# Optimization experiments

Hardware: AMD Instinct MI355X
Metric: run time of the kernel (lower is better)

The kernel has to match this reference:

```python
import jax, jax.numpy as jnp
import numpy as np

B, C, H, W = 4, 256, 64, 64
DQK = C // 8

def setup_inputs() -> dict:
    key = jax.random.key(0)
    ks = jax.random.split(key, 8)
    s = 0.05
    return {
        "x": jax.random.normal(ks[0], (B, C, H, W), jnp.float32),
        "Wq": jax.random.normal(ks[1], (DQK, C), jnp.float32) * s,
        "bq": jax.random.normal(ks[2], (DQK,), jnp.float32) * s,
        "Wk": jax.random.normal(ks[3], (DQK, C), jnp.float32) * s,
        "bk": jax.random.normal(ks[4], (DQK,), jnp.float32) * s,
        "Wv": jax.random.normal(ks[5], (C, C), jnp.float32) * s,
        "bv": jax.random.normal(ks[6], (C,), jnp.float32) * s,
        "gamma": jax.random.normal(ks[7], (1,), jnp.float32) * s,
    }

def reference(x, Wq, bq, Wk, bk, Wv, bv, gamma):
    b, c, h, w = x.shape
    n = h * w
    xf = x.reshape(b, c, n)                                  # (B,C,N)
    # 1x1 convs == per-pixel linear projections
    q = jnp.einsum('dc,bcn->bnd', Wq, xf) + bq               # (B,N,Dqk)
    k = jnp.einsum('dc,bcn->bdn', Wk, xf) + bk[:, None]      # (B,Dqk,N)
    v = jnp.einsum('dc,bcn->bdn', Wv, xf) + bv[:, None]      # (B,C,N)
    energy = jnp.einsum('bnd,bdm->bnm', q, k)                # (B,N,N) — NO 1/sqrt(d) scaling, matching source
    attn = jax.nn.softmax(energy, axis=-1)
    # out[b,c,m] = sum_n v[b,c,n] * attn[m,n]  (bmm(value, attn^T))
    out = jnp.einsum('bcn,bmn->bcm', v, attn).reshape(b, c, h, w)
    return gamma * out + x
```

## Files before the change

### kernel.cpp

```cpp
#include <hip/hip_runtime.h>


#define BATCH 4
#define CH    256
#define NPIX  4096
#define DQKD  32

typedef __attribute__((ext_vector_type(8))) short bf16x8;
typedef __attribute__((ext_vector_type(4))) float f32x4;

__device__ __forceinline__ unsigned pk2(float a, float b) {
    return (__float_as_uint(a) >> 16) | (__float_as_uint(b) & 0xffff0000u);
}

__global__ __launch_bounds__(256) void proj_kernel(
    const float* __restrict__ x,
    const float* __restrict__ Wq, const float* __restrict__ bq,
    const float* __restrict__ Wk, const float* __restrict__ bk,
    const float* __restrict__ Wv, const float* __restrict__ bv,
    ushort* __restrict__ qb, ushort* __restrict__ kb, ushort* __restrict__ vb)
{
    __shared__ float w_lds[32][256];
    __shared__ float b_lds[32];
    const int tid = threadIdx.x;
    const int n0  = blockIdx.x * 256;
    const int dt  = blockIdx.y;
    const int b   = blockIdx.z;

    const float* W; const float* bias;
    if (dt == 0)      { W = Wq;                              bias = bq; }
    else if (dt == 1) { W = Wk;                              bias = bk; }
    else              { W = Wv + (size_t)(dt - 2) * 32 * CH; bias = bv + (dt - 2) * 32; }

    {
        const float4* w4 = (const float4*)W;
        float4* l4 = (float4*)&w_lds[0][0];
        #pragma unroll
        for (int i = 0; i < 8; ++i) l4[tid + 256 * i] = w4[tid + 256 * i];
        if (tid < 32) b_lds[tid] = bias[tid];
    }
    __syncthreads();

    const int tn = tid & 63;
    const int td = tid >> 6;
    const int n  = n0 + tn * 4;

    float acc[8][4];
    #pragma unroll
    for (int i = 0; i < 8; ++i) {
        float bb = b_lds[td * 8 + i];
        #pragma unroll
        for (int j = 0; j < 4; ++j) acc[i][j] = bb;
    }

    const float* xb = x + (size_t)b * CH * NPIX + n;
    for (int c0 = 0; c0 < CH; c0 += 8) {
        float xr[8][4];
        #pragma unroll
        for (int cc = 0; cc < 8; ++cc) {
            float4 xv = *(const float4*)(xb + (size_t)(c0 + cc) * NPIX);
            xr[cc][0] = xv.x; xr[cc][1] = xv.y; xr[cc][2] = xv.z; xr[cc][3] = xv.w;
        }
        #pragma unroll
        for (int i = 0; i < 8; ++i) {
            #pragma unroll
            for (int h = 0; h < 2; ++h) {
                float4 w4 = *(const float4*)&w_lds[td * 8 + i][c0 + 4 * h];
                float wr[4] = {w4.x, w4.y, w4.z, w4.w};
                #pragma unroll
                for (int cc = 0; cc < 4; ++cc)
                    #pragma unroll
                    for (int j = 0; j < 4; ++j)
                        acc[i][j] = fmaf(wr[cc], xr[4 * h + cc][j], acc[i][j]);
            }
        }
    }

    if (dt == 0 || dt == 1) {
        ushort* dst = (dt == 0) ? qb : kb;
        const float sc = (dt == 0) ? 1.4426950408889634f : 1.0f;
        #pragma unroll
        for (int j = 0; j < 4; ++j) {
            uint4 u;
            u.x = pk2(acc[0][j] * sc, acc[1][j] * sc);
            u.y = pk2(acc[2][j] * sc, acc[3][j] * sc);
            u.z = pk2(acc[4][j] * sc, acc[5][j] * sc);
            u.w = pk2(acc[6][j] * sc, acc[7][j] * sc);
            *(uint4*)(dst + ((size_t)b * NPIX + n + j) * DQKD + td * 8) = u;
        }
    } else {
        const int cbase = (dt - 2) * 32 + td * 8;
        #pragma unroll
        for (int i = 0; i < 8; ++i) {
            uint2 u;
            u.x = pk2(acc[i][0], acc[i][1]);
            u.y = pk2(acc[i][2], acc[i][3]);
            *(uint2*)(vb + ((size_t)b * CH + cbase + i) * NPIX + n) = u;
        }
    }
}

__global__ __launch_bounds__(512, 2) void attn_kernel(
    const ushort* __restrict__ Qb, const ushort* __restrict__ Kb,
    const ushort* __restrict__ Vb, const float* __restrict__ x,
    const float* __restrict__ gamma_p, float* __restrict__ out)
{
    __shared__ char  p_lds[64 * 1024];
    __shared__ float l_lds[8][64];
    __shared__ float linv_lds[64];

    const int tid  = threadIdx.x;
    const int lane = tid & 63;
    const int wv   = tid >> 6;
    const int l15  = lane & 15, g = lane >> 4;
    const unsigned swz = (unsigned)(l15 & 7) << 4;

    int bid  = blockIdx.x;
    int xcd  = bid & 7, slot = bid >> 3;
    int b    = xcd >> 1;
    int qt   = slot + 32 * (xcd & 1);
    const int m0 = qt * 64;

    bf16x8 qf[4];
    #pragma unroll
    for (int qc = 0; qc < 4; ++qc)
        qf[qc] = *(const bf16x8*)(Qb + ((size_t)b * NPIX + m0 + 16 * qc + l15) * DQKD + 8 * g);

    const ushort* kbase = Kb + ((size_t)b * NPIX + 64 * wv + l15) * DQKD + 8 * g;

    const int qh = wv >> 2;
    const int cg = wv & 3;
    const ushort* vbase = Vb + ((size_t)(b * CH + 64 * cg) + l15) * NPIX + 8 * g;

    f32x4 acc[2][4];
    #pragma unroll
    for (int q2 = 0; q2 < 2; ++q2)
        #pragma unroll
        for (int ct = 0; ct < 4; ++ct) acc[q2][ct] = (f32x4){0.f, 0.f, 0.f, 0.f};
    float l_run[4] = {0.f, 0.f, 0.f, 0.f};

    const f32x4 z4 = {0.f, 0.f, 0.f, 0.f};

    bf16x8 kc[4];
    #pragma unroll
    for (int t = 0; t < 4; ++t)
        kc[t] = *(const bf16x8*)(kbase + (size_t)(16 * t) * DQKD);

    #pragma unroll 1
    for (int kt = 0; kt < NPIX; kt += 512) {
        #pragma unroll
        for (int t = 0; t < 4; ++t) {
            #pragma unroll
            for (int qc = 0; qc < 4; ++qc) {
                f32x4 st = __builtin_amdgcn_mfma_f32_16x16x32_bf16(kc[t], qf[qc], z4, 0, 0, 0);
                float p0 = exp2f(st[0]);
                float p1 = exp2f(st[1]);
                float p2 = exp2f(st[2]);
                float p3 = exp2f(st[3]);
                l_run[qc] += (p0 + p1) + (p2 + p3);
                unsigned row = 16 * qc + l15;
                unsigned off = row * 1024 + ((128u * wv + 32u * t + 8u * g) ^ swz);
                uint2 u; u.x = pk2(p0, p1); u.y = pk2(p2, p3);
                *(uint2*)(p_lds + off) = u;
            }
        }
        __syncthreads();

        {
            int ktn = (kt + 512) & (NPIX - 1);
            #pragma unroll
            for (int t = 0; t < 4; ++t)
                kc[t] = *(const bf16x8*)(kbase + (size_t)(ktn + 16 * t) * DQKD);
        }

        {
            bf16x8 vb0[3][4];
            #pragma unroll
            for (int p = 0; p < 2; ++p)
                #pragma unroll
                for (int ct = 0; ct < 4; ++ct)
                    vb0[p][ct] = *(const bf16x8*)(vbase + (size_t)(16 * ct) * NPIX + kt + 32 * p);

            #pragma unroll
            for (int ks = 0; ks < 16; ++ks) {
                if (ks + 2 < 16) {
                    #pragma unroll
                    for (int ct = 0; ct < 4; ++ct)
                        vb0[(ks + 2) % 3][ct] =
                            *(const bf16x8*)(vbase + (size_t)(16 * ct) * NPIX + kt + 32 * (ks + 2));
                }
                #pragma unroll
                for (int q2 = 0; q2 < 2; ++q2) {
                    unsigned row = 32 * qh + 16 * q2 + l15;
                    unsigned off = row * 1024 + ((64u * ks + 16u * g) ^ swz);
                    bf16x8 pa = *(const bf16x8*)(p_lds + off);
                    #pragma unroll
                    for (int ct = 0; ct < 4; ++ct)
                        acc[q2][ct] = __builtin_amdgcn_mfma_f32_16x16x32_bf16(
                            pa, vb0[ks % 3][ct], acc[q2][ct], 0, 0, 0);
                }
            }
        }
        __syncthreads();
    }

    #pragma unroll
    for (int qc = 0; qc < 4; ++qc) {
        l_run[qc] += __shfl_xor(l_run[qc], 16);
        l_run[qc] += __shfl_xor(l_run[qc], 32);
        if (g == 0) l_lds[wv][16 * qc + l15] = l_run[qc];
    }
    __syncthreads();
    if (tid < 64) {
        float s = 0.f;
        #pragma unroll
        for (int w = 0; w < 8; ++w) s += l_lds[w][tid];
        linv_lds[tid] = 1.0f / s;
    }
    __syncthreads();

    const float gm = gamma_p[0];
    #pragma unroll
    for (int q2 = 0; q2 < 2; ++q2) {
        float4 li = *(const float4*)&linv_lds[32 * qh + 16 * q2 + 4 * g];
        #pragma unroll
        for (int ct = 0; ct < 4; ++ct) {
            size_t o = ((size_t)b * CH + 64 * cg + 16 * ct + l15) * NPIX
                     + m0 + 32 * qh + 16 * q2 + 4 * g;
            float4 xv = *(const float4*)(x + o);
            float4 ov;
            ov.x = fmaf(gm, acc[q2][ct][0] * li.x, xv.x);
            ov.y = fmaf(gm, acc[q2][ct][1] * li.y, xv.y);
            ov.z = fmaf(gm, acc[q2][ct][2] * li.z, xv.z);
            ov.w = fmaf(gm, acc[q2][ct][3] * li.w, xv.w);
            *(float4*)(out + o) = ov;
        }
    }
}

extern "C" void kernel_launch(void* const* d_in, const int* in_sizes, int n_in,
                              void* d_out, int out_size, void* d_ws, size_t ws_size,
                              hipStream_t stream)
{
    (void)in_sizes; (void)n_in; (void)out_size; (void)ws_size;
    const float* x  = (const float*)d_in[0];
    const float* Wq = (const float*)d_in[1];
    const float* bq = (const float*)d_in[2];
    const float* Wk = (const float*)d_in[3];
    const float* bk = (const float*)d_in[4];
    const float* Wv = (const float*)d_in[5];
    const float* bv = (const float*)d_in[6];
    const float* gm = (const float*)d_in[7];
    float* out = (float*)d_out;

    ushort* qw = (ushort*)d_ws;
    ushort* kw = qw + (size_t)BATCH * NPIX * DQKD;
    ushort* vw = kw + (size_t)BATCH * NPIX * DQKD;

    dim3 g1(NPIX / 256, 10, BATCH);
    proj_kernel<<<g1, 256, 0, stream>>>(x, Wq, bq, Wk, bk, Wv, bv, qw, kw, vw);

    attn_kernel<<<dim3(256), 512, 0, stream>>>(qw, kw, vw, x, gm, out);
}
```

Measured before the change: 267.5 us.

## Halve attention query tile to 32 rows, doubling blocks and occupancy

Cuts the per-block query tile from 64 to 32 rows, halving the P buffer in LDS and the accumulator registers, and launches 512 blocks with launch bounds asking for 4 blocks per CU instead of 2. The K fragments are now loaded inside each iteration rather than prefetched across iterations, and the V loads use a two-slot double buffer instead of a three-slot ring. The goal is more resident waves to hide latency and spread work over all CUs. The cost is that every K and V tile is streamed from memory twice as often per query row, since each block reuses them across fewer queries.

```diff
diff --git a/kernel.cpp b/kernel.cpp
--- a/kernel.cpp
+++ b/kernel.cpp
@@ -100,14 +100,14 @@
     }
 }
 
-__global__ __launch_bounds__(512, 2) void attn_kernel(
+__global__ __launch_bounds__(512, 4) void attn_kernel(
     const ushort* __restrict__ Qb, const ushort* __restrict__ Kb,
     const ushort* __restrict__ Vb, const float* __restrict__ x,
     const float* __restrict__ gamma_p, float* __restrict__ out)
 {
-    __shared__ char  p_lds[64 * 1024];
-    __shared__ float l_lds[8][64];
-    __shared__ float linv_lds[64];
+    __shared__ char  p_lds[32 * 1024];
+    __shared__ float l_lds[8][32];
+    __shared__ float linv_lds[32];
 
     const int tid  = threadIdx.x;
     const int lane = tid & 63;
@@ -118,12 +118,12 @@
     int bid  = blockIdx.x;
     int xcd  = bid & 7, slot = bid >> 3;
     int b    = xcd >> 1;
-    int qt   = slot + 32 * (xcd & 1);
-    const int m0 = qt * 64;
-
-    bf16x8 qf[4];
-    #pragma unroll
-    for (int qc = 0; qc < 4; ++qc)
+    int qt   = slot + 64 * (xcd & 1);
+    const int m0 = qt * 32;
+
+    bf16x8 qf[2];
+    #pragma unroll
+    for (int qc = 0; qc < 2; ++qc)
         qf[qc] = *(const bf16x8*)(Qb + ((size_t)b * NPIX + m0 + 16 * qc + l15) * DQKD + 8 * g);
 
     const ushort* kbase = Kb + ((size_t)b * NPIX + 64 * wv + l15) * DQKD + 8 * g;
@@ -132,86 +132,79 @@
     const int cg = wv & 3;
     const ushort* vbase = Vb + ((size_t)(b * CH + 64 * cg) + l15) * NPIX + 8 * g;
 
-    f32x4 acc[2][4];
-    #pragma unroll
-    for (int q2 = 0; q2 < 2; ++q2)
-        #pragma unroll
-        for (int ct = 0; ct < 4; ++ct) acc[q2][ct] = (f32x4){0.f, 0.f, 0.f, 0.f};
-    float l_run[4] = {0.f, 0.f, 0.f, 0.f};
+    f32x4 acc[4];
+    #pragma unroll
+    for (int ct = 0; ct < 4; ++ct) acc[ct] = (f32x4){0.f, 0.f, 0.f, 0.f};
+    float l_run[2] = {0.f, 0.f};
 
     const f32x4 z4 = {0.f, 0.f, 0.f, 0.f};
-
-    bf16x8 kc[4];
-    #pragma unroll
-    for (int t = 0; t < 4; ++t)
-        kc[t] = *(const bf16x8*)(kbase + (size_t)(16 * t) * DQKD);
 
     #pragma unroll 1
     for (int kt = 0; kt < NPIX; kt += 512) {
-        #pragma unroll
-        for (int t = 0; t < 4; ++t) {
-            #pragma unroll
-            for (int qc = 0; qc < 4; ++qc) {
-                f32x4 st = __builtin_amdgcn_mfma_f32_16x16x32_bf16(kc[t], qf[qc], z4, 0, 0, 0);
-                float p0 = exp2f(st[0]);
-                float p1 = exp2f(st[1]);
-                float p2 = exp2f(st[2]);
-                float p3 = exp2f(st[3]);
-                l_run[qc] += (p0 + p1) + (p2 + p3);
-                unsigned row = 16 * qc + l15;
-                unsigned off = row * 1024 + ((128u * wv + 32u * t + 8u * g) ^ swz);
-                uint2 u; u.x = pk2(p0, p1); u.y = pk2(p2, p3);
-                *(uint2*)(p_lds + off) = u;
+        {
+            bf16x8 kf[4];
+            #pragma unroll
+            for (int t = 0; t < 4; ++t)
+                kf[t] = *(const bf16x8*)(kbase + (size_t)(kt + 16 * t) * DQKD);
+            #pragma unroll
+            for (int t = 0; t < 4; ++t) {
+                #pragma unroll
+                for (int qc = 0; qc < 2; ++qc) {
+                    f32x4 st = __builtin_amdgcn_mfma_f32_16x16x32_bf16(kf[t], qf[qc], z4, 0, 0, 0);
+                    float p0 = exp2f(st[0]);
+                    float p1 = exp2f(st[1]);
+                    float p2 = exp2f(st[2]);
+                    float p3 = exp2f(st[3]);
+                    l_run[qc] += (p0 + p1) + (p2 + p3);
+                    unsigned row = 16 * qc + l15;
+                    unsigned off = row * 1024 + ((128u * wv + 32u * t + 8u * g) ^ swz);
+                    uint2 u; u.x = pk2(p0, p1); u.y = pk2(p2, p3);
+                    *(uint2*)(p_lds + off) = u;
+                }
             }
         }
         __syncthreads();
 
         {
-            int ktn = (kt + 512) & (NPIX - 1);
-            #pragma unroll
-            for (int t = 0; t < 4; ++t)
-                kc[t] = *(const bf16x8*)(kbase + (size_t)(ktn + 16 * t) * DQKD);
-        }
-
-        {
-            bf16x8 vb0[3][4];
-            #pragma unroll
-            for (int p = 0; p < 2; ++p)
-                #pragma unroll
-                for (int ct = 0; ct < 4; ++ct)
-                    vb0[p][ct] = *(const bf16x8*)(vbase + (size_t)(16 * ct) * NPIX + kt + 32 * p);
-
-            #pragma unroll
-            for (int ks = 0; ks < 16; ++ks) {
-                if (ks + 2 < 16) {
-                    #pragma unroll
-                    for (int ct = 0; ct < 4; ++ct)
-                        vb0[(ks + 2) % 3][ct] =
-                            *(const bf16x8*)(vbase + (size_t)(16 * ct) * NPIX + kt + 32 * (ks + 2));
-                }
-                #pragma unroll
-                for (int q2 = 0; q2 < 2; ++q2) {
-                    unsigned row = 32 * qh + 16 * q2 + l15;
-                    unsigned off = row * 1024 + ((64u * ks + 16u * g) ^ swz);
-                    bf16x8 pa = *(const bf16x8*)(p_lds + off);
-                    #pragma unroll
-                    for (int ct = 0; ct < 4; ++ct)
-                        acc[q2][ct] = __builtin_amdgcn_mfma_f32_16x16x32_bf16(
-                            pa, vb0[ks % 3][ct], acc[q2][ct], 0, 0, 0);
-                }
-            }
+            bf16x8 va[4], vn[4];
+            #pragma unroll
+            for (int ct = 0; ct < 4; ++ct)
+                va[ct] = *(const bf16x8*)(vbase + (size_t)(16 * ct) * NPIX + kt);
+
+#define PV_STEP(CUR, NXT, KS)                                                   \
+            {                                                                   \
+                if ((KS) < 15) {                                                \
+                    _Pragma("unroll")                                           \
+                    for (int ct = 0; ct < 4; ++ct)                              \
+                        NXT[ct] = *(const bf16x8*)(vbase + (size_t)(16 * ct) * NPIX \
+                                                   + kt + 32 * ((KS) + 1));     \
+                }                                                               \
+                unsigned off = (16u * qh + l15) * 1024u + ((64u * (KS) + 16u * g) ^ swz); \
+                bf16x8 pa = *(const bf16x8*)(p_lds + off);                      \
+                _Pragma("unroll")                                               \
+                for (int ct = 0; ct < 4; ++ct)                                  \
+                    acc[ct] = __builtin_amdgcn_mfma_f32_16x16x32_bf16(          \
+                        pa, CUR[ct], acc[ct], 0, 0, 0);                         \
+            }
+
+            #pragma unroll
+            for (int ks2 = 0; ks2 < 8; ++ks2) {
+                PV_STEP(va, vn, 2 * ks2);
+                PV_STEP(vn, va, 2 * ks2 + 1);
+            }
+#undef PV_STEP
         }
         __syncthreads();
     }
 
     #pragma unroll
-    for (int qc = 0; qc < 4; ++qc) {
+    for (int qc = 0; qc < 2; ++qc) {
         l_run[qc] += __shfl_xor(l_run[qc], 16);
         l_run[qc] += __shfl_xor(l_run[qc], 32);
         if (g == 0) l_lds[wv][16 * qc + l15] = l_run[qc];
     }
     __syncthreads();
-    if (tid < 64) {
+    if (tid < 32) {
         float s = 0.f;
         #pragma unroll
         for (int w = 0; w < 8; ++w) s += l_lds[w][tid];
@@ -220,21 +213,18 @@
     __syncthreads();
 
     const float gm = gamma_p[0];
-    #pragma unroll
-    for (int q2 = 0; q2 < 2; ++q2) {
-        float4 li = *(const float4*)&linv_lds[32 * qh + 16 * q2 + 4 * g];
-        #pragma unroll
-        for (int ct = 0; ct < 4; ++ct) {
-            size_t o = ((size_t)b * CH + 64 * cg + 16 * ct + l15) * NPIX
-                     + m0 + 32 * qh + 16 * q2 + 4 * g;
-            float4 xv = *(const float4*)(x + o);
-            float4 ov;
-            ov.x = fmaf(gm, acc[q2][ct][0] * li.x, xv.x);
-            ov.y = fmaf(gm, acc[q2][ct][1] * li.y, xv.y);
-            ov.z = fmaf(gm, acc[q2][ct][2] * li.z, xv.z);
-            ov.w = fmaf(gm, acc[q2][ct][3] * li.w, xv.w);
-            *(float4*)(out + o) = ov;
-        }
+    float4 li = *(const float4*)&linv_lds[16 * qh + 4 * g];
+    #pragma unroll
+    for (int ct = 0; ct < 4; ++ct) {
+        size_t o = ((size_t)b * CH + 64 * cg + 16 * ct + l15) * NPIX
+                 + m0 + 16 * qh + 4 * g;
+        float4 xv = *(const float4*)(x + o);
+        float4 ov;
+        ov.x = fmaf(gm, acc[ct][0] * li.x, xv.x);
+        ov.y = fmaf(gm, acc[ct][1] * li.y, xv.y);
+        ov.z = fmaf(gm, acc[ct][2] * li.z, xv.z);
+        ov.w = fmaf(gm, acc[ct][3] * li.w, xv.w);
+        *(float4*)(out + o) = ov;
     }
 }
 
@@ -260,5 +250,5 @@
     dim3 g1(NPIX / 256, 10, BATCH);
     proj_kernel<<<g1, 256, 0, stream>>>(x, Wq, bq, Wk, bk, Wv, bv, qw, kw, vw);
 
-    attn_kernel<<<dim3(256), 512, 0, stream>>>(qw, kw, vw, x, gm, out);
-}
+    attn_kernel<<<dim3(512), 512, 0, stream>>>(qw, kw, vw, x, gm, out);
+}
```

Result: slower. 360.5 us (+34.8%).
